# Optimization experiments

Measured on AMD Instinct MI355X. Metric: run time of the kernel, lower is better.

## Reference

```python
import jax, jax.numpy as jnp
import numpy as np

HEAD_DIM = 64  # hidden_dim 1024 // heads_num 16


def setup_inputs() -> dict:
    key = jax.random.key(0)
    ks = jax.random.split(key, 5)
    B, S, H = 2, 4096, 1024
    std = 1.0 / np.sqrt(H)
    return {
        "x": jax.random.normal(ks[0], (B, S, H), jnp.float32),
        "Wq": jax.random.normal(ks[1], (H, H), jnp.float32) * std,
        "bq": jnp.zeros((H,), jnp.float32),
        "Wk": jax.random.normal(ks[2], (H, H), jnp.float32) * std,
        "bk": jnp.zeros((H,), jnp.float32),
        "Wv": jax.random.normal(ks[3], (H, H), jnp.float32) * std,
        "bv": jnp.zeros((H,), jnp.float32),
        "Wo": jax.random.normal(ks[4], (H, H), jnp.float32) * std,
        "bo": jnp.zeros((H,), jnp.float32),
    }


def reference(x, Wq, bq, Wk, bk, Wv, bv, Wo, bo):
    # Linear projections (torch Linear: x @ W^T + b)
    q = jnp.einsum("bsh,oh->bso", x, Wq) + bq
    k = jnp.einsum("bsh,oh->bso", x, Wk) + bk
    v = jnp.einsum("bsh,oh->bso", x, Wv) + bv
    # all_to_all is identity on a single device (world size 1)
    scale = jnp.float32(HEAD_DIM) ** 0.5
    # Faithful to source: attention over the FULL hidden dim (no head split),
    # full [B, S, S] score matrix.
    scores = jnp.einsum("bqh,bkh->bqk", q, k) / scale
    weights = jax.nn.softmax(scores, axis=-1)
    attn = jnp.einsum("bqk,bkh->bqh", weights, v)
    out = jnp.einsum("bsh,oh->bso", attn, Wo) + bo
    return out
```

## Files before the change

### kernel.cpp

```cpp
#include <hip/hip_runtime.h>
#include <stdint.h>


typedef __bf16 bf16x8 __attribute__((ext_vector_type(8)));
typedef float  f32x4  __attribute__((ext_vector_type(4)));

__device__ __forceinline__ unsigned short f32_to_bf16_rne(float f) {
    uint32_t u = __builtin_bit_cast(uint32_t, f);
    uint32_t r = (u + 0x7FFFu + ((u >> 16) & 1u)) >> 16;
    return (unsigned short)r;
}

#define BM 128
#define BN 128
#define BK 64

__global__ __launch_bounds__(256) void cvt_all(
    const float* __restrict__ x,
    const float* __restrict__ Wq, const float* __restrict__ Wk,
    const float* __restrict__ Wo, const float* __restrict__ Wv,
    const float* __restrict__ bv, const float* __restrict__ bo,
    unsigned short* __restrict__ x16, unsigned short* __restrict__ w16,
    float* __restrict__ rsum, float* __restrict__ bfinal)
{
    const int b = blockIdx.x, tid = threadIdx.x;
    if (b < 8192) {
        int i = (b * 256 + tid) * 4;
        float4 v = *(const float4*)(x + i);
        ushort4 o;
        o.x = f32_to_bf16_rne(v.x); o.y = f32_to_bf16_rne(v.y);
        o.z = f32_to_bf16_rne(v.z); o.w = f32_to_bf16_rne(v.w);
        *(ushort4*)(x16 + i) = o;
    } else if (b < 11264) {
        int bb = b - 8192;
        int which = bb >> 10;
        const float* src = which == 0 ? Wq : which == 1 ? Wk : Wo;
        int i = ((bb & 1023) * 256 + tid) * 4;
        float4 v = *(const float4*)(src + i);
        ushort4 o;
        o.x = f32_to_bf16_rne(v.x); o.y = f32_to_bf16_rne(v.y);
        o.z = f32_to_bf16_rne(v.z); o.w = f32_to_bf16_rne(v.w);
        *(ushort4*)(w16 + (size_t)which * 1048576 + i) = o;
    } else if (b < 11520) {
        __shared__ unsigned short tl[64 * 68];
        int t = b - 11264, tr = t >> 4, tc = t & 15;
        #pragma unroll
        for (int it = 0; it < 4; ++it) {
            int r  = it * 16 + (tid >> 4);
            int c0 = (tid & 15) * 4;
            float4 v = *(const float4*)(Wv + (size_t)(tr * 64 + r) * 1024 + tc * 64 + c0);
            tl[(c0 + 0) * 68 + r] = f32_to_bf16_rne(v.x);
            tl[(c0 + 1) * 68 + r] = f32_to_bf16_rne(v.y);
            tl[(c0 + 2) * 68 + r] = f32_to_bf16_rne(v.z);
            tl[(c0 + 3) * 68 + r] = f32_to_bf16_rne(v.w);
        }
        __syncthreads();
        #pragma unroll
        for (int it = 0; it < 4; ++it) {
            int c  = it * 16 + (tid >> 4);
            int r0 = (tid & 15) * 4;
            ushort4 o;
            o.x = tl[c * 68 + r0 + 0]; o.y = tl[c * 68 + r0 + 1];
            o.z = tl[c * 68 + r0 + 2]; o.w = tl[c * 68 + r0 + 3];
            *(ushort4*)(w16 + (size_t)3 * 1048576 + (size_t)(tc * 64 + c) * 1024 + tr * 64 + r0) = o;
        }
    } else if (b < 11536) {
        int bb = b - 11520;
        int lane = tid & 63, wv_ = tid >> 6;
        int rowBase = bb * 64 + wv_ * 16;
        for (int rr = 0; rr < 16; ++rr) {
            int row = rowBase + rr;
            float partial = 0.f;
            #pragma unroll
            for (int t2 = 0; t2 < 16; ++t2) {
                int h = t2 * 64 + lane;
                partial += Wo[(size_t)row * 1024 + h] * bv[h];
            }
            #pragma unroll
            for (int off = 32; off > 0; off >>= 1)
                partial += __shfl_xor(partial, off, 64);
            if (lane == 0) bfinal[row] = bo[row] + partial;
        }
    } else {
        int i = ((b - 11536) * 256 + tid) * 4;
        *(float4*)(rsum + i) = float4{0.f, 0.f, 0.f, 0.f};
    }
}

__device__ __forceinline__ void gemm_core(
    const unsigned short* __restrict__ Ab,
    const unsigned short* __restrict__ Bb,
    unsigned short* ldsA, unsigned short* ldsB,
    int mBase, int nBase, int lane, int wave, int K, f32x4 (&acc)[4][4])
{
    const int quad = lane >> 4;
    const int l16  = lane & 15;
    const int wr   = wave >> 1;
    const int wc   = wave & 1;

    for (int k0 = 0; k0 < K; k0 += BK) {
        #pragma unroll
        for (int i = 0; i < 4; ++i) {
            int base = (i * 4 + wave) * 64;
            int s    = base + lane;
            int row  = s >> 3;
            int col  = ((s ^ (s >> 3)) & 7) * 8;
            __builtin_amdgcn_global_load_lds(
                (const __attribute__((address_space(1))) void*)(Ab + (size_t)(mBase + row) * K + (size_t)(k0 + col)),
                (__attribute__((address_space(3))) void*)(&ldsA[base * 8]),
                16, 0, 0);
        }
        #pragma unroll
        for (int i = 0; i < 4; ++i) {
            int base = (i * 4 + wave) * 64;
            int s    = base + lane;
            int row  = s >> 3;
            int col  = ((s ^ (s >> 3)) & 7) * 8;
            __builtin_amdgcn_global_load_lds(
                (const __attribute__((address_space(1))) void*)(Bb + (size_t)(nBase + row) * K + (size_t)(k0 + col)),
                (__attribute__((address_space(3))) void*)(&ldsB[base * 8]),
                16, 0, 0);
        }
        __syncthreads();

        #pragma unroll
        for (int kk = 0; kk < 2; ++kk) {
            bf16x8 af[4], bfv[4];
            #pragma unroll
            for (int mi = 0; mi < 4; ++mi) {
                int r = wr * 64 + mi * 16 + l16;
                int c = kk * 4 + quad;
                af[mi] = *(const bf16x8*)(&ldsA[r * BK + (((c ^ r) & 7) << 3)]);
            }
            #pragma unroll
            for (int ni = 0; ni < 4; ++ni) {
                int r = wc * 64 + ni * 16 + l16;
                int c = kk * 4 + quad;
                bfv[ni] = *(const bf16x8*)(&ldsB[r * BK + (((c ^ r) & 7) << 3)]);
            }
            #pragma unroll
            for (int mi = 0; mi < 4; ++mi)
                #pragma unroll
                for (int ni = 0; ni < 4; ++ni)
                    acc[mi][ni] = __builtin_amdgcn_mfma_f32_16x16x32_bf16(
                        af[mi], bfv[ni], acc[mi][ni], 0, 0, 0);
        }
        __syncthreads();
    }
}

template <int MODE>
__global__ __launch_bounds__(256) void gemm_bt(
    const unsigned short* __restrict__ A,
    const unsigned short* __restrict__ Bt,
    void* __restrict__ C,
    const float* __restrict__ b0, float* __restrict__ rowsum,
    float alpha, int M, int N, int K,
    long long aZ, long long bZ, long long cZ)
{
    __shared__ unsigned short ldsA[BM * BK];
    __shared__ unsigned short ldsB[BN * BK];

    const int NB = gridDim.x, MBt = gridDim.y;
    int l  = blockIdx.x + gridDim.x * (blockIdx.y + gridDim.y * blockIdx.z);
    int xcd = l & 7;
    int t   = l >> 3;
    int MBX = MBt >> 1;
    int NBX = NB >> 2;
    int mbl = t % MBX;
    int r1  = t / MBX;
    int nbi = r1 % NBX;
    int zb  = r1 / NBX;
    int mb  = (xcd >> 2) * MBX + mbl;
    int nb  = (xcd & 3) * NBX + nbi;

    const unsigned short* Ab = A  + (size_t)zb * aZ;
    const unsigned short* Bb = Bt + (size_t)zb * bZ;

    const int tid  = threadIdx.x;
    const int lane = tid & 63;
    const int wave = tid >> 6;
    const int quad = lane >> 4;
    const int l16  = lane & 15;
    const int wr   = wave >> 1;
    const int wc   = wave & 1;
    const int mBase = mb * BM;
    const int nBase = nb * BN;

    f32x4 acc[4][4] = {};
    gemm_core(Ab, Bb, ldsA, ldsB, mBase, nBase, lane, wave, K, acc);

    if (MODE == 1) {
        unsigned short* Cz = (unsigned short*)C + (size_t)zb * cZ;
        #pragma unroll
        for (int mi = 0; mi < 4; ++mi)
            #pragma unroll
            for (int ni = 0; ni < 4; ++ni) {
                int col = nBase + wc * 64 + ni * 16 + l16;
                float b = b0 ? b0[col] : 0.f;
                #pragma unroll
                for (int r = 0; r < 4; ++r) {
                    int row = mBase + wr * 64 + mi * 16 + quad * 4 + r;
                    Cz[(size_t)row * N + col] = f32_to_bf16_rne(acc[mi][ni][r] + b);
                }
            }
    } else if (MODE == 3) {
        unsigned short* Pz = (unsigned short*)C + (size_t)zb * cZ;
        float* rs = rowsum + (size_t)zb * M;
        #pragma unroll
        for (int mi = 0; mi < 4; ++mi) {
            #pragma unroll
            for (int r = 0; r < 4; ++r) {
                int row = mBase + wr * 64 + mi * 16 + quad * 4 + r;
                float e[4];
                float partial = 0.f;
                #pragma unroll
                for (int ni = 0; ni < 4; ++ni) {
                    e[ni] = __expf(acc[mi][ni][r] * alpha);
                    partial += e[ni];
                }
                #pragma unroll
                for (int ni = 0; ni < 4; ++ni) {
                    int col = nBase + wc * 64 + ni * 16 + l16;
                    Pz[(size_t)row * N + col] = f32_to_bf16_rne(e[ni]);
                }
                #pragma unroll
                for (int off = 1; off < 16; off <<= 1)
                    partial += __shfl_xor(partial, off, 64);
                if (l16 == 0) atomicAdd(&rs[row], partial);
            }
        }
    }
}

__global__ __launch_bounds__(256) void gemm_qkf(
    const unsigned short* __restrict__ x16,
    const unsigned short* __restrict__ w16,
    unsigned short* __restrict__ q16,
    unsigned short* __restrict__ k16,
    unsigned short* __restrict__ F16,
    const float* __restrict__ bq, const float* __restrict__ bk)
{
    __shared__ unsigned short ldsA[BM * BK];
    __shared__ unsigned short ldsB[BN * BK];

    int l   = blockIdx.x;
    int idx = (l & 7) * 136 + (l >> 3);

    const unsigned short *Ab, *Bb;
    unsigned short* Cb;
    const float* bias;
    int mBase, nBase;
    if (idx < 1024) {
        int role = idx >> 9;
        int s    = idx & 511;
        mBase = (s >> 3) * BM; nBase = (s & 7) * BN;
        Ab = x16; Bb = w16 + (size_t)role * 1048576;
        Cb = role ? k16 : q16; bias = role ? bk : bq;
    } else {
        int f = idx - 1024;
        mBase = (f >> 3) * BM; nBase = (f & 7) * BN;
        Ab = w16 + (size_t)2 * 1048576;
        Bb = w16 + (size_t)3 * 1048576;
        Cb = F16; bias = nullptr;
    }

    const int tid  = threadIdx.x;
    const int lane = tid & 63;
    const int wave = tid >> 6;
    const int quad = lane >> 4;
    const int l16  = lane & 15;
    const int wr   = wave >> 1;
    const int wc   = wave & 1;

    f32x4 acc[4][4] = {};
    gemm_core(Ab, Bb, ldsA, ldsB, mBase, nBase, lane, wave, 1024, acc);

    #pragma unroll
    for (int mi = 0; mi < 4; ++mi)
        #pragma unroll
        for (int ni = 0; ni < 4; ++ni) {
            int col = nBase + wc * 64 + ni * 16 + l16;
            float b = bias ? bias[col] : 0.f;
            #pragma unroll
            for (int r = 0; r < 4; ++r) {
                int row = mBase + wr * 64 + mi * 16 + quad * 4 + r;
                Cb[(size_t)row * 1024 + col] = f32_to_bf16_rne(acc[mi][ni][r] + b);
            }
        }
}

template <int MODE, int BMt, int BNt>
__global__ __launch_bounds__(512) void gemm8p(
    const unsigned short* __restrict__ A,
    const unsigned short* __restrict__ Bt,
    void* __restrict__ C,
    const float* __restrict__ b0, float* __restrict__ rowsum,
    float alpha, int M, int N, int K,
    long long aZ, long long bZ, long long cZ,
    int MBt, int NB)
{
    constexpr int RW  = BMt / 2;
    constexpr int CW  = BNt / 4;
    constexpr int MI  = RW / 16;
    constexpr int NI  = CW / 16;
    constexpr int NPH = MI / 2;
    constexpr int BL  = (BNt * 64 / 512) / 8;
    constexpr int NWT = BL + NPH - 1;

    __shared__ __align__(16) unsigned short ldsA[2][BMt * 64];
    __shared__ __align__(16) unsigned short ldsB[2][BNt * 64];

    const int l   = blockIdx.x;
    const int xcd = l & 7;
    const int t   = l >> 3;
    const int MBX = MBt >> 1;
    const int NBX = NB >> 2;
    const int mbl = t % MBX;
    const int r1  = t / MBX;
    const int nbi = r1 % NBX;
    const int zb  = r1 / NBX;
    const int mb  = (xcd >> 2) * MBX + mbl;
    const int nb  = (xcd & 3) * NBX + nbi;

    const unsigned short* Ab = A  + (size_t)zb * aZ;
    const unsigned short* Bb = Bt + (size_t)zb * bZ;

    const int tid  = threadIdx.x;
    const int lane = tid & 63;
    const int wave = tid >> 6;
    const int quad = lane >> 4;
    const int l16  = lane & 15;
    const int wr   = wave >> 2;
    const int wc   = wave & 3;
    const int mBase = mb * BMt;
    const int nBase = nb * BNt;
    const int NT    = K >> 6;

    const int aRow0 = ((wave & 4) ? RW : 0) + (wave & 3) * 8;

    auto stageA = [&](int p, int kt, int q) {
        const int rowbase = aRow0 + q * 32;
        const int row = rowbase + (lane >> 3);
        const int col = (((lane & 7) ^ row) & 7) << 3;
        __builtin_amdgcn_global_load_lds(
            (const __attribute__((address_space(1))) void*)(
                Ab + (size_t)(mBase + row) * K + (size_t)((kt << 6) + col)),
            (__attribute__((address_space(3))) void*)(&ldsA[p][rowbase * 64]),
            16, 0, 0);
    };
    auto stageB = [&](int p, int kt) {
        #pragma unroll
        for (int i = 0; i < BL; ++i) {
            const int g   = wave * BL + i;
            const int row = (g << 3) + (lane >> 3);
            const int col = (((lane & 7) ^ row) & 7) << 3;
            __builtin_amdgcn_global_load_lds(
                (const __attribute__((address_space(1))) void*)(
                    Bb + (size_t)(nBase + row) * K + (size_t)((kt << 6) + col)),
                (__attribute__((address_space(3))) void*)(&ldsB[p][g << 9]),
                16, 0, 0);
        }
    };

    bf16x8 bf[NI][2];
    bf16x8 af[2][2];
    auto ldB = [&](int p) {
        #pragma unroll
        for (int n2 = 0; n2 < NI; ++n2)
            #pragma unroll
            for (int kk = 0; kk < 2; ++kk) {
                const int r = wc * CW + n2 * 16 + l16;
                const int c = kk * 4 + quad;
                bf[n2][kk] = *(const bf16x8*)&ldsB[p][r * 64 + (((c ^ r) & 7) << 3)];
            }
    };
    auto ldA = [&](int p, int q) {
        #pragma unroll
        for (int m2 = 0; m2 < 2; ++m2)
            #pragma unroll
            for (int kk = 0; kk < 2; ++kk) {
                const int r = wr * RW + (q * 2 + m2) * 16 + l16;
                const int c = kk * 4 + quad;
                af[m2][kk] = *(const bf16x8*)&ldsA[p][r * 64 + (((c ^ r) & 7) << 3)];
            }
    };

    f32x4 acc[MI][NI] = {};

    stageB(0, 0);
    #pragma unroll
    for (int q = 0; q < NPH; ++q) stageA(0, 0, q);
    if (NT > 1) {
        stageB(1, 1);
        #pragma unroll
        for (int q = 0; q < NPH - 1; ++q) stageA(1, 1, q);
        asm volatile("s_waitcnt vmcnt(%0)" :: "n"(NWT) : "memory");
    } else {
        asm volatile("s_waitcnt vmcnt(0)" ::: "memory");
    }
    __builtin_amdgcn_s_barrier();

    for (int kt = 0; kt < NT; ++kt) {
        const int p = kt & 1;
        #pragma unroll
        for (int q = 0; q < NPH; ++q) {
            if (q == 0) ldB(p);
            ldA(p, q);
            if (q == 0) {
                if (kt + 1 < NT) stageA(p ^ 1, kt + 1, NPH - 1);
            } else if (q == 1) {
                if (kt + 2 < NT) { stageB(p, kt + 2); stageA(p, kt + 2, 0); }
            } else {
                if (kt + 2 < NT) stageA(p, kt + 2, q - 1);
            }
            if (q == NPH - 1) {
                if (kt + 2 < NT) {
                    asm volatile("s_waitcnt vmcnt(%0)" :: "n"(NWT) : "memory");
                } else if (kt + 1 < NT) {
                    asm volatile("s_waitcnt vmcnt(0)" ::: "memory");
                }
            }
            __builtin_amdgcn_s_barrier();
            asm volatile("s_waitcnt lgkmcnt(0)" ::: "memory");
            __builtin_amdgcn_sched_barrier(0);
            __builtin_amdgcn_s_setprio(1);
            #pragma unroll
            for (int m2 = 0; m2 < 2; ++m2)
                #pragma unroll
                for (int n2 = 0; n2 < NI; ++n2)
                    #pragma unroll
                    for (int kk = 0; kk < 2; ++kk)
                        acc[q * 2 + m2][n2] = __builtin_amdgcn_mfma_f32_16x16x32_bf16(
                            af[m2][kk], bf[n2][kk], acc[q * 2 + m2][n2], 0, 0, 0);
            __builtin_amdgcn_s_setprio(0);
            __builtin_amdgcn_s_barrier();
        }
    }

    {
        float* Cz = (float*)C + (size_t)zb * cZ;
        const float* rs = rowsum + (size_t)zb * M;
        #pragma unroll
        for (int mi = 0; mi < MI; ++mi) {
            #pragma unroll
            for (int r = 0; r < 4; ++r) {
                const int row = mBase + wr * RW + mi * 16 + quad * 4 + r;
                const float inv = 1.f / rs[row];
                #pragma unroll
                for (int ni = 0; ni < NI; ++ni) {
                    const int col = nBase + wc * CW + ni * 16 + l16;
                    Cz[(size_t)row * N + col] = acc[mi][ni][r] * inv + b0[col];
                }
            }
        }
    }
}

extern "C" void kernel_launch(void* const* d_in, const int* in_sizes, int n_in,
                              void* d_out, int out_size, void* d_ws, size_t ws_size,
                              hipStream_t stream)
{
    const float* x  = (const float*)d_in[0];
    const float* Wq = (const float*)d_in[1];
    const float* bq = (const float*)d_in[2];
    const float* Wk = (const float*)d_in[3];
    const float* bk = (const float*)d_in[4];
    const float* Wv = (const float*)d_in[5];
    const float* bv = (const float*)d_in[6];
    const float* Wo = (const float*)d_in[7];
    const float* bo = (const float*)d_in[8];
    float* out = (float*)d_out;

    const int S = 4096, H = 1024, Bsz = 2;
    const int M = Bsz * S;

    char* p = (char*)d_ws;
    auto alloc = [&](size_t bytes) -> char* {
        char* r = p; p += (bytes + 255) & ~(size_t)255; return r;
    };
    unsigned short* w16  = (unsigned short*)alloc((size_t)4 * H * H * 2);
    unsigned short* F16  = (unsigned short*)alloc((size_t)H * H * 2);
    unsigned short* q16  = (unsigned short*)alloc((size_t)M * H * 2);
    unsigned short* k16  = (unsigned short*)alloc((size_t)M * H * 2);
    unsigned short* vot16= (unsigned short*)alloc((size_t)Bsz * H * S * 2);
    float*          rsum = (float*)alloc((size_t)M * 4);
    float*          bfin = (float*)alloc((size_t)H * 4);
    char* region = alloc((size_t)Bsz * S * S * 2);
    unsigned short* x16 = (unsigned short*)region;
    unsigned short* p16 = (unsigned short*)region;

    cvt_all<<<11544, 256, 0, stream>>>(x, Wq, Wk, Wo, Wv, bv, bo,
                                       x16, w16, rsum, bfin);

    gemm_qkf<<<1088, 256, 0, stream>>>(x16, w16, q16, k16, F16, bq, bk);

    gemm_bt<1><<<dim3(S / BN, H / BM, 2), 256, 0, stream>>>(
        F16, x16, vot16, nullptr, nullptr, 1.f, H, S, 1024,
        0, (long long)S * H, (long long)H * S);

    gemm_bt<3><<<dim3(S / BN, S / BM, 2), 256, 0, stream>>>(
        q16, k16, p16, nullptr, rsum, 0.125f, S, S, 1024,
        (long long)S * H, (long long)S * H, (long long)S * S);

    gemm8p<6, 128, 256><<<256, 512, 0, stream>>>(
        p16, vot16, out, bfin, rsum, 1.f, S, H, 4096,
        (long long)S * S, (long long)H * S, (long long)S * H, 32, 4);
}
```

Measured before the change: 369.3 us.

## Fold Wq·Wk^T into one weight matrix to skip the K projection

Result: slower. 385.6 us (+4.4%).

```diff
diff --git a/kernel.cpp b/kernel.cpp
--- a/kernel.cpp
+++ b/kernel.cpp
@@ -11,6 +11,10 @@
     return (unsigned short)r;
 }
 
+__device__ __forceinline__ float bf16_to_f32(unsigned short s) {
+    return __builtin_bit_cast(float, (uint32_t)s << 16);
+}
+
 #define BM 128
 #define BN 128
 #define BK 64
@@ -19,9 +23,11 @@
     const float* __restrict__ x,
     const float* __restrict__ Wq, const float* __restrict__ Wk,
     const float* __restrict__ Wo, const float* __restrict__ Wv,
+    const float* __restrict__ bq, const float* __restrict__ bk,
     const float* __restrict__ bv, const float* __restrict__ bo,
     unsigned short* __restrict__ x16, unsigned short* __restrict__ w16,
-    float* __restrict__ rsum, float* __restrict__ bfinal)
+    float* __restrict__ rsum, float* __restrict__ bfinal,
+    float* __restrict__ g0, float* __restrict__ u, float* __restrict__ bqbk)
 {
     const int b = blockIdx.x, tid = threadIdx.x;
     if (b < 8192) {
@@ -31,24 +37,25 @@
         o.x = f32_to_bf16_rne(v.x); o.y = f32_to_bf16_rne(v.y);
         o.z = f32_to_bf16_rne(v.z); o.w = f32_to_bf16_rne(v.w);
         *(ushort4*)(x16 + i) = o;
-    } else if (b < 11264) {
-        int bb = b - 8192;
-        int which = bb >> 10;
-        const float* src = which == 0 ? Wq : which == 1 ? Wk : Wo;
-        int i = ((bb & 1023) * 256 + tid) * 4;
-        float4 v = *(const float4*)(src + i);
+    } else if (b < 9216) {
+        int i = ((b - 8192) * 256 + tid) * 4;
+        float4 v = *(const float4*)(Wo + i);
         ushort4 o;
         o.x = f32_to_bf16_rne(v.x); o.y = f32_to_bf16_rne(v.y);
         o.z = f32_to_bf16_rne(v.z); o.w = f32_to_bf16_rne(v.w);
-        *(ushort4*)(w16 + (size_t)which * 1048576 + i) = o;
-    } else if (b < 11520) {
+        *(ushort4*)(w16 + (size_t)2 * 1048576 + i) = o;
+    } else if (b < 9984) {
         __shared__ unsigned short tl[64 * 68];
-        int t = b - 11264, tr = t >> 4, tc = t & 15;
+        int t = b - 9216;
+        int which = t >> 8;
+        const float* src = which == 0 ? Wq : which == 1 ? Wk : Wv;
+        size_t slot = which == 0 ? 0 : which == 1 ? 1 : 3;
+        int tile = t & 255, tr = tile >> 4, tc = tile & 15;
         #pragma unroll
         for (int it = 0; it < 4; ++it) {
             int r  = it * 16 + (tid >> 4);
             int c0 = (tid & 15) * 4;
-            float4 v = *(const float4*)(Wv + (size_t)(tr * 64 + r) * 1024 + tc * 64 + c0);
+            float4 v = *(const float4*)(src + (size_t)(tr * 64 + r) * 1024 + tc * 64 + c0);
             tl[(c0 + 0) * 68 + r] = f32_to_bf16_rne(v.x);
             tl[(c0 + 1) * 68 + r] = f32_to_bf16_rne(v.y);
             tl[(c0 + 2) * 68 + r] = f32_to_bf16_rne(v.z);
@@ -62,10 +69,10 @@
             ushort4 o;
             o.x = tl[c * 68 + r0 + 0]; o.y = tl[c * 68 + r0 + 1];
             o.z = tl[c * 68 + r0 + 2]; o.w = tl[c * 68 + r0 + 3];
-            *(ushort4*)(w16 + (size_t)3 * 1048576 + (size_t)(tc * 64 + c) * 1024 + tr * 64 + r0) = o;
-        }
-    } else if (b < 11536) {
-        int bb = b - 11520;
+            *(ushort4*)(w16 + slot * 1048576 + (size_t)(tc * 64 + c) * 1024 + tr * 64 + r0) = o;
+        }
+    } else if (b < 10000) {
+        int bb = b - 9984;
         int lane = tid & 63, wv_ = tid >> 6;
         int rowBase = bb * 64 + wv_ * 16;
         for (int rr = 0; rr < 16; ++rr) {
@@ -81,8 +88,30 @@
                 partial += __shfl_xor(partial, off, 64);
             if (lane == 0) bfinal[row] = bo[row] + partial;
         }
+    } else if (b < 10004) {
+        int j = (b - 10000) * 256 + tid;
+        float acc = 0.f;
+        #pragma unroll 8
+        for (int h = 0; h < 1024; ++h) acc += bq[h] * Wk[(size_t)h * 1024 + j];
+        g0[j] = acc;
+    } else if (b < 10008) {
+        int j = (b - 10004) * 256 + tid;
+        float acc = 0.f;
+        #pragma unroll 8
+        for (int h = 0; h < 1024; ++h) acc += bk[h] * Wq[(size_t)h * 1024 + j];
+        u[j] = acc;
+    } else if (b == 10008) {
+        float partial = bq[tid] * bk[tid] + bq[tid + 256] * bk[tid + 256]
+                      + bq[tid + 512] * bk[tid + 512] + bq[tid + 768] * bk[tid + 768];
+        #pragma unroll
+        for (int off = 32; off > 0; off >>= 1)
+            partial += __shfl_xor(partial, off, 64);
+        __shared__ float red[4];
+        if ((tid & 63) == 0) red[tid >> 6] = partial;
+        __syncthreads();
+        if (tid == 0) bqbk[0] = red[0] + red[1] + red[2] + red[3];
     } else {
-        int i = ((b - 11536) * 256 + tid) * 4;
+        int i = (b - 10009) * 1024 + tid * 4;
         *(float4*)(rsum + i) = float4{0.f, 0.f, 0.f, 0.f};
     }
 }
@@ -147,6 +176,116 @@
         }
         __syncthreads();
     }
+}
+
+__global__ __launch_bounds__(256) void gemm_gf(
+    const unsigned short* __restrict__ w16,
+    const unsigned short* __restrict__ x16,
+    unsigned short* __restrict__ Gt16, unsigned short* __restrict__ F16,
+    const float* __restrict__ u, const float* __restrict__ bqbk,
+    float* __restrict__ rowadd)
+{
+    const int l = blockIdx.x, tid = threadIdx.x;
+    if (l < 128) {
+        __shared__ unsigned short ldsA[BM * BK];
+        __shared__ unsigned short ldsB[BN * BK];
+        const unsigned short *Ab, *Bb;
+        unsigned short* Cb;
+        int f;
+        if (l < 64) { f = l;      Ab = w16 + (size_t)1 * 1048576; Bb = w16;                        Cb = Gt16; }
+        else        { f = l - 64; Ab = w16 + (size_t)2 * 1048576; Bb = w16 + (size_t)3 * 1048576; Cb = F16;  }
+        int mBase = (f >> 3) * BM, nBase = (f & 7) * BN;
+
+        const int lane = tid & 63, wave = tid >> 6;
+        const int quad = lane >> 4, l16 = lane & 15;
+        const int wr = wave >> 1, wc = wave & 1;
+
+        f32x4 acc[4][4] = {};
+        gemm_core(Ab, Bb, ldsA, ldsB, mBase, nBase, lane, wave, 1024, acc);
+
+        #pragma unroll
+        for (int mi = 0; mi < 4; ++mi)
+            #pragma unroll
+            for (int ni = 0; ni < 4; ++ni) {
+                int col = nBase + wc * 64 + ni * 16 + l16;
+                #pragma unroll
+                for (int r = 0; r < 4; ++r) {
+                    int row = mBase + wr * 64 + mi * 16 + quad * 4 + r;
+                    Cb[(size_t)row * 1024 + col] = f32_to_bf16_rne(acc[mi][ni][r]);
+                }
+            }
+    } else {
+        int rb = l - 128;
+        int lane = tid & 63, w = tid >> 6;
+        float bb0 = bqbk[0];
+        for (int rr = 0; rr < 16; ++rr) {
+            int row = rb * 64 + w * 16 + rr;
+            float partial = 0.f;
+            #pragma unroll
+            for (int t2 = 0; t2 < 16; ++t2) {
+                int h = t2 * 64 + lane;
+                partial += bf16_to_f32(x16[(size_t)row * 1024 + h]) * u[h];
+            }
+            #pragma unroll
+            for (int off = 32; off > 0; off >>= 1)
+                partial += __shfl_xor(partial, off, 64);
+            if (lane == 0) rowadd[row] = partial + bb0;
+        }
+    }
+}
+
+__global__ __launch_bounds__(256) void gemm_qgv(
+    const unsigned short* __restrict__ x16,
+    const unsigned short* __restrict__ Gt16,
+    const unsigned short* __restrict__ F16,
+    const float* __restrict__ g0,
+    unsigned short* __restrict__ qg16,
+    unsigned short* __restrict__ vot16)
+{
+    __shared__ unsigned short ldsA[BM * BK];
+    __shared__ unsigned short ldsB[BN * BK];
+
+    int l   = blockIdx.x;
+    int idx = (l & 7) * 128 + (l >> 3);
+
+    const unsigned short *Ab, *Bb;
+    unsigned short* Cb;
+    const float* bias;
+    int mBase, nBase, Cstride;
+    if (idx < 512) {
+        mBase = (idx >> 3) * BM; nBase = (idx & 7) * BN;
+        Ab = x16; Bb = Gt16; Cb = qg16; bias = g0; Cstride = 1024;
+    } else {
+        int v = idx - 512;
+        int zb = v >> 8, t2 = v & 255;
+        mBase = (t2 >> 5) * BM; nBase = (t2 & 31) * BN;
+        Ab = F16; Bb = x16 + (size_t)zb * 4096 * 1024;
+        Cb = vot16 + (size_t)zb * 1024 * 4096; bias = nullptr; Cstride = 4096;
+    }
+
+    const int tid  = threadIdx.x;
+    const int lane = tid & 63;
+    const int wave = tid >> 6;
+    const int quad = lane >> 4;
+    const int l16  = lane & 15;
+    const int wr   = wave >> 1;
+    const int wc   = wave & 1;
+
+    f32x4 acc[4][4] = {};
+    gemm_core(Ab, Bb, ldsA, ldsB, mBase, nBase, lane, wave, 1024, acc);
+
+    #pragma unroll
+    for (int mi = 0; mi < 4; ++mi)
+        #pragma unroll
+        for (int ni = 0; ni < 4; ++ni) {
+            int col = nBase + wc * 64 + ni * 16 + l16;
+            float b = bias ? bias[col] : 0.f;
+            #pragma unroll
+            for (int r = 0; r < 4; ++r) {
+                int row = mBase + wr * 64 + mi * 16 + quad * 4 + r;
+                Cb[(size_t)row * Cstride + col] = f32_to_bf16_rne(acc[mi][ni][r] + b);
+            }
+        }
 }
 
 template <int MODE>
@@ -190,33 +329,21 @@
     f32x4 acc[4][4] = {};
     gemm_core(Ab, Bb, ldsA, ldsB, mBase, nBase, lane, wave, K, acc);
 
-    if (MODE == 1) {
-        unsigned short* Cz = (unsigned short*)C + (size_t)zb * cZ;
-        #pragma unroll
-        for (int mi = 0; mi < 4; ++mi)
-            #pragma unroll
-            for (int ni = 0; ni < 4; ++ni) {
-                int col = nBase + wc * 64 + ni * 16 + l16;
-                float b = b0 ? b0[col] : 0.f;
-                #pragma unroll
-                for (int r = 0; r < 4; ++r) {
-                    int row = mBase + wr * 64 + mi * 16 + quad * 4 + r;
-                    Cz[(size_t)row * N + col] = f32_to_bf16_rne(acc[mi][ni][r] + b);
-                }
-            }
-    } else if (MODE == 3) {
+    if (MODE == 3) {
         unsigned short* Pz = (unsigned short*)C + (size_t)zb * cZ;
         float* rs = rowsum + (size_t)zb * M;
+        const float* raz = b0 + (size_t)zb * M;
         #pragma unroll
         for (int mi = 0; mi < 4; ++mi) {
             #pragma unroll
             for (int r = 0; r < 4; ++r) {
                 int row = mBase + wr * 64 + mi * 16 + quad * 4 + r;
+                float ra = raz[row];
                 float e[4];
                 float partial = 0.f;
                 #pragma unroll
                 for (int ni = 0; ni < 4; ++ni) {
-                    e[ni] = __expf(acc[mi][ni][r] * alpha);
+                    e[ni] = __expf((acc[mi][ni][r] + ra) * alpha);
                     partial += e[ni];
                 }
                 #pragma unroll
@@ -231,63 +358,6 @@
             }
         }
     }
-}
-
-__global__ __launch_bounds__(256) void gemm_qkf(
-    const unsigned short* __restrict__ x16,
-    const unsigned short* __restrict__ w16,
-    unsigned short* __restrict__ q16,
-    unsigned short* __restrict__ k16,
-    unsigned short* __restrict__ F16,
-    const float* __restrict__ bq, const float* __restrict__ bk)
-{
-    __shared__ unsigned short ldsA[BM * BK];
-    __shared__ unsigned short ldsB[BN * BK];
-
-    int l   = blockIdx.x;
-    int idx = (l & 7) * 136 + (l >> 3);
-
-    const unsigned short *Ab, *Bb;
-    unsigned short* Cb;
-    const float* bias;
-    int mBase, nBase;
-    if (idx < 1024) {
-        int role = idx >> 9;
-        int s    = idx & 511;
-        mBase = (s >> 3) * BM; nBase = (s & 7) * BN;
-        Ab = x16; Bb = w16 + (size_t)role * 1048576;
-        Cb = role ? k16 : q16; bias = role ? bk : bq;
-    } else {
-        int f = idx - 1024;
-        mBase = (f >> 3) * BM; nBase = (f & 7) * BN;
-        Ab = w16 + (size_t)2 * 1048576;
-        Bb = w16 + (size_t)3 * 1048576;
-        Cb = F16; bias = nullptr;
-    }
-
-    const int tid  = threadIdx.x;
-    const int lane = tid & 63;
-    const int wave = tid >> 6;
-    const int quad = lane >> 4;
-    const int l16  = lane & 15;
-    const int wr   = wave >> 1;
-    const int wc   = wave & 1;
-
-    f32x4 acc[4][4] = {};
-    gemm_core(Ab, Bb, ldsA, ldsB, mBase, nBase, lane, wave, 1024, acc);
-
-    #pragma unroll
-    for (int mi = 0; mi < 4; ++mi)
-        #pragma unroll
-        for (int ni = 0; ni < 4; ++ni) {
-            int col = nBase + wc * 64 + ni * 16 + l16;
-            float b = bias ? bias[col] : 0.f;
-            #pragma unroll
-            for (int r = 0; r < 4; ++r) {
-                int row = mBase + wr * 64 + mi * 16 + quad * 4 + r;
-                Cb[(size_t)row * 1024 + col] = f32_to_bf16_rne(acc[mi][ni][r] + b);
-            }
-        }
 }
 
 template <int MODE, int BMt, int BNt>
@@ -479,28 +549,29 @@
     auto alloc = [&](size_t bytes) -> char* {
         char* r = p; p += (bytes + 255) & ~(size_t)255; return r;
     };
-    unsigned short* w16  = (unsigned short*)alloc((size_t)4 * H * H * 2);
-    unsigned short* F16  = (unsigned short*)alloc((size_t)H * H * 2);
-    unsigned short* q16  = (unsigned short*)alloc((size_t)M * H * 2);
-    unsigned short* k16  = (unsigned short*)alloc((size_t)M * H * 2);
-    unsigned short* vot16= (unsigned short*)alloc((size_t)Bsz * H * S * 2);
-    float*          rsum = (float*)alloc((size_t)M * 4);
-    float*          bfin = (float*)alloc((size_t)H * 4);
-    char* region = alloc((size_t)Bsz * S * S * 2);
-    unsigned short* x16 = (unsigned short*)region;
-    unsigned short* p16 = (unsigned short*)region;
-
-    cvt_all<<<11544, 256, 0, stream>>>(x, Wq, Wk, Wo, Wv, bv, bo,
-                                       x16, w16, rsum, bfin);
-
-    gemm_qkf<<<1088, 256, 0, stream>>>(x16, w16, q16, k16, F16, bq, bk);
-
-    gemm_bt<1><<<dim3(S / BN, H / BM, 2), 256, 0, stream>>>(
-        F16, x16, vot16, nullptr, nullptr, 1.f, H, S, 1024,
-        0, (long long)S * H, (long long)H * S);
+    unsigned short* w16   = (unsigned short*)alloc((size_t)4 * H * H * 2);
+    unsigned short* F16   = (unsigned short*)alloc((size_t)H * H * 2);
+    unsigned short* Gt16  = (unsigned short*)alloc((size_t)H * H * 2);
+    unsigned short* qg16  = (unsigned short*)alloc((size_t)M * H * 2);
+    unsigned short* vot16 = (unsigned short*)alloc((size_t)Bsz * H * S * 2);
+    unsigned short* x16   = (unsigned short*)alloc((size_t)M * H * 2);
+    float*          rsum  = (float*)alloc((size_t)M * 4);
+    float*          bfin  = (float*)alloc((size_t)H * 4);
+    float*          g0    = (float*)alloc((size_t)H * 4);
+    float*          uvec  = (float*)alloc((size_t)H * 4);
+    float*          bqbk  = (float*)alloc(256);
+    float*          rowadd= (float*)alloc((size_t)M * 4);
+    unsigned short* p16   = (unsigned short*)alloc((size_t)Bsz * S * S * 2);
+
+    cvt_all<<<10017, 256, 0, stream>>>(x, Wq, Wk, Wo, Wv, bq, bk, bv, bo,
+                                       x16, w16, rsum, bfin, g0, uvec, bqbk);
+
+    gemm_gf<<<256, 256, 0, stream>>>(w16, x16, Gt16, F16, uvec, bqbk, rowadd);
+
+    gemm_qgv<<<1024, 256, 0, stream>>>(x16, Gt16, F16, g0, qg16, vot16);
 
     gemm_bt<3><<<dim3(S / BN, S / BM, 2), 256, 0, stream>>>(
-        q16, k16, p16, nullptr, rsum, 0.125f, S, S, 1024,
+        qg16, x16, p16, rowadd, rsum, 0.125f, S, S, 1024,
         (long long)S * H, (long long)S * H, (long long)S * S);
 
     gemm8p<6, 128, 256><<<256, 512, 0, stream>>>(
```
